# Kernel optimization log

Measured on AMD Instinct MI355X. Metric: run time of the kernel, lower is better.

Reference implementation:

```python
import jax, jax.numpy as jnp
import numpy as np

KQ = 512
NEG = -1e9


def setup_inputs() -> dict:
    key = jax.random.key(0)
    k1, k2, k3, k4, k5 = jax.random.split(key, 5)
    B, NQ, NK, D, V, O = 16, 1024, 2048, 512, 512, 256
    return {
        "keys": jax.random.normal(k1, (B, NK, D), dtype=jnp.float32),
        "queries": jax.random.normal(k2, (B, NQ, D), dtype=jnp.float32),
        "values": jax.random.normal(k3, (B, NK, V), dtype=jnp.float32),
        "mask": jax.random.randint(k4, (B, NQ, NK), 0, 2, dtype=jnp.int32),
        "W_resize": jax.random.normal(k5, (O, V), dtype=jnp.float32) * (1.0 / np.sqrt(V)),
        "b_resize": jnp.zeros((O,), dtype=jnp.float32),
    }


def reference(keys, queries, values, mask, W_resize, b_resize):
    # score: scaled dot product  [B, NQ, NK]
    logits = jnp.einsum("bqd,bkd->bqk", queries, keys) / jnp.sqrt(jnp.float32(KQ))
    logits = jnp.where(mask == 0, jnp.float32(NEG), logits)
    attn = jax.nn.softmax(logits, axis=-1)
    # context: [B, NQ, V]
    context = jnp.einsum("bqk,bkv->bqv", attn, values)
    # resize to out_size
    context = jnp.einsum("bqv,ov->bqo", context, W_resize) + b_resize
    return context
```

## Files before the change

### kernel.cpp

```cpp
#include <hip/hip_runtime.h>

#define BB   16
#define NQ   1024
#define NK   2048
#define DD   512
#define VV   512
#define OO   256
#define SCALE 0.044194173824159216f

typedef __attribute__((ext_vector_type(4))) float f32x4;
typedef __attribute__((ext_vector_type(8))) short s16x8;

#define AS1(p) ((const __attribute__((address_space(1))) void*)(p))
#define AS3(p) ((__attribute__((address_space(3))) void*)(p))

__device__ __forceinline__ unsigned short f2bf(float f) {
  unsigned u = __float_as_uint(f);
  u += 0x7fffu + ((u >> 16) & 1u);
  return (unsigned short)(u >> 16);
}
__device__ __forceinline__ float bf2f(unsigned short b) {
  return __uint_as_float(((unsigned)b) << 16);
}

#define MFMA16(a, b, c) __builtin_amdgcn_mfma_f32_16x16x32_bf16(a, b, c, 0, 0, 0)

__device__ __forceinline__ void gemm_bt_core(
    const unsigned short* __restrict__ Abase,
    const unsigned short* __restrict__ Bbase,
    int K,
    unsigned short* As, unsigned short* Bs,
    f32x4 acc[4][4])
{
  const int t = threadIdx.x;
  const int w = t >> 6;
  const int l = t & 63;
  const int srow = l >> 2;
  const int scol = (l & 3) * 8;
  const int r0 = (w * 2 + 0) * 16 + srow;
  const int r1 = (w * 2 + 1) * 16 + srow;
  const int lds0 = (w * 2 + 0) * 512 + l * 8;
  const int lds1 = (w * 2 + 1) * 512 + l * 8;
  const int wm = (w >> 1) * 64;
  const int wn = (w & 1) * 64;
  const int lm = l & 15;
  const int lq = l >> 4;

  for (int kt = 0; kt < K; kt += 32) {
    __builtin_amdgcn_global_load_lds(AS1(Abase + (size_t)r0 * K + kt + scol), AS3(As + lds0), 16, 0, 0);
    __builtin_amdgcn_global_load_lds(AS1(Abase + (size_t)r1 * K + kt + scol), AS3(As + lds1), 16, 0, 0);
    __builtin_amdgcn_global_load_lds(AS1(Bbase + (size_t)r0 * K + kt + scol), AS3(Bs + lds0), 16, 0, 0);
    __builtin_amdgcn_global_load_lds(AS1(Bbase + (size_t)r1 * K + kt + scol), AS3(Bs + lds1), 16, 0, 0);
    __syncthreads();
    s16x8 af[4], bfr[4];
    #pragma unroll
    for (int i = 0; i < 4; ++i) {
      af[i]  = *(const s16x8*)(As + (wm + i * 16 + lm) * 32 + lq * 8);
      bfr[i] = *(const s16x8*)(Bs + (wn + i * 16 + lm) * 32 + lq * 8);
    }
    #pragma unroll
    for (int mi = 0; mi < 4; ++mi)
      #pragma unroll
      for (int ni = 0; ni < 4; ++ni)
        acc[mi][ni] = MFMA16(af[mi], bfr[ni], acc[mi][ni]);
    __syncthreads();
  }
}


#define CS_STRIDE 136

__global__ __launch_bounds__(256)
void qkvw_kernel(const unsigned short* __restrict__ Qb,
                 const unsigned short* __restrict__ Kb,
                 const unsigned short* __restrict__ Vb,
                 const unsigned short* __restrict__ Wb,
                 const int* __restrict__ mask,
                 unsigned short* __restrict__ P,
                 unsigned short* __restrict__ VWt,
                 float* __restrict__ sums)
{
  __shared__ unsigned short smem[128 * CS_STRIDE];
  unsigned short* As = smem;
  unsigned short* Bs = smem + 4096;
  unsigned short* Cs = smem;
  const int bid = blockIdx.x;
  const int t = threadIdx.x, w = t >> 6, l = t & 63;
  const int wm = (w >> 1) * 64, wn = (w & 1) * 64;
  const int lm = l & 15, lq = l >> 4;
  const int trow = t >> 4, tcol = (t & 15) * 8;

  f32x4 acc[4][4];
  #pragma unroll
  for (int i = 0; i < 4; ++i)
    #pragma unroll
    for (int j = 0; j < 4; ++j) acc[i][j] = (f32x4){0.f, 0.f, 0.f, 0.f};

  if (bid < 2048) {
    const int b  = bid >> 7;
    const int tm = (bid >> 4) & 7;
    const int tn = bid & 15;

    gemm_bt_core(Qb + ((size_t)b * NQ + tm * 128) * DD,
                 Kb + ((size_t)b * NK + tn * 128) * DD, DD, As, Bs, acc);

    #pragma unroll
    for (int mi = 0; mi < 4; ++mi)
      #pragma unroll
      for (int ni = 0; ni < 4; ++ni)
        #pragma unroll
        for (int r = 0; r < 4; ++r)
          Cs[(wm + mi * 16 + lq * 4 + r) * CS_STRIDE + wn + ni * 16 + lm] =
              f2bf(acc[mi][ni][r] * SCALE);
    __syncthreads();

    #pragma unroll
    for (int it = 0; it < 8; ++it) {
      const int row = it * 16 + trow;
      const int gq = tm * 128 + row;
      const size_t gbase = ((size_t)b * NQ + gq) * NK + tn * 128 + tcol;
      s16x8 v = *(const s16x8*)(Cs + row * CS_STRIDE + tcol);
      const int4 m0 = *(const int4*)(mask + gbase);
      const int4 m1 = *(const int4*)(mask + gbase + 4);
      float e[8];
      e[0] = m0.x ? __expf(bf2f((unsigned short)v[0])) : 0.f;
      e[1] = m0.y ? __expf(bf2f((unsigned short)v[1])) : 0.f;
      e[2] = m0.z ? __expf(bf2f((unsigned short)v[2])) : 0.f;
      e[3] = m0.w ? __expf(bf2f((unsigned short)v[3])) : 0.f;
      e[4] = m1.x ? __expf(bf2f((unsigned short)v[4])) : 0.f;
      e[5] = m1.y ? __expf(bf2f((unsigned short)v[5])) : 0.f;
      e[6] = m1.z ? __expf(bf2f((unsigned short)v[6])) : 0.f;
      e[7] = m1.w ? __expf(bf2f((unsigned short)v[7])) : 0.f;
      float sp = 0.f;
      #pragma unroll
      for (int j = 0; j < 8; ++j) sp += e[j];
      #pragma unroll
      for (int off = 8; off > 0; off >>= 1) sp += __shfl_down(sp, off, 16);
      if ((t & 15) == 0) atomicAdd(&sums[(size_t)b * NQ + gq], sp);
      s16x8 o;
      #pragma unroll
      for (int j = 0; j < 8; ++j) o[j] = (short)f2bf(e[j]);
      *(s16x8*)(P + gbase) = o;
    }
  } else {
    const int vid = bid - 2048;
    const int b  = vid >> 5;
    const int kt = (vid >> 1) & 15;
    const int ot = vid & 1;

    gemm_bt_core(Vb + ((size_t)b * NK + kt * 128) * VV,
                 Wb + (size_t)ot * 128 * VV, VV, As, Bs, acc);

    #pragma unroll
    for (int mi = 0; mi < 4; ++mi)
      #pragma unroll
      for (int ni = 0; ni < 4; ++ni)
        #pragma unroll
        for (int r = 0; r < 4; ++r)
          Cs[(wn + ni * 16 + lm) * CS_STRIDE + wm + mi * 16 + lq * 4 + r] =
              f2bf(acc[mi][ni][r]);
    __syncthreads();

    #pragma unroll
    for (int it = 0; it < 8; ++it) {
      const int orow = it * 16 + trow;
      s16x8 v = *(const s16x8*)(Cs + orow * CS_STRIDE + tcol);
      *(s16x8*)(VWt + ((size_t)b * OO + ot * 128 + orow) * NK + kt * 128 + tcol) = v;
    }
  }
}

#define PW_STRIDE 132
__global__ __launch_bounds__(256)
void pvw_kernel(const unsigned short* __restrict__ P,
                const unsigned short* __restrict__ VWt,
                const float* __restrict__ sums,
                const float* __restrict__ bias,
                float* __restrict__ out)
{
  const int ot = blockIdx.x;
  const int qt = blockIdx.y;
  const int b  = blockIdx.z;
  __shared__ unsigned short smem[24576];
  __shared__ float Ls[64];

  const int t = threadIdx.x, w = t >> 6, l = t & 63;
  const int wr = w >> 1, wc = w & 1;
  const int lm = l & 15, lq = l >> 4;
  if (t < 64) Ls[t] = 1.0f / sums[(size_t)b * NQ + qt * 64 + t];

  f32x4 acc[2][4];
  #pragma unroll
  for (int i = 0; i < 2; ++i)
    #pragma unroll
    for (int j = 0; j < 4; ++j) acc[i][j] = (f32x4){0.f, 0.f, 0.f, 0.f};

  const unsigned short* Abase = P   + ((size_t)b * NQ + qt * 64) * NK;
  const unsigned short* Bbase = VWt + ((size_t)b * OO + ot * 128) * NK;

  const int srow = t >> 3;
  const int ssc  = (((t & 7) ^ (srow & 7)) << 3);

#define PV_STAGE(buf, k0v) do {                                                            \
    unsigned short* As_ = smem + (buf) * 12288;                                            \
    unsigned short* Bs_ = As_ + 4096;                                                      \
    const int k0_ = (k0v);                                                                 \
    __builtin_amdgcn_global_load_lds(AS1(Abase + (size_t)(srow     ) * NK + k0_ + ssc), AS3(As_ +        t * 8), 16, 0, 0); \
    __builtin_amdgcn_global_load_lds(AS1(Abase + (size_t)(srow + 32) * NK + k0_ + ssc), AS3(As_ + 2048 + t * 8), 16, 0, 0); \
    __builtin_amdgcn_global_load_lds(AS1(Bbase + (size_t)(srow     ) * NK + k0_ + ssc), AS3(Bs_ +        t * 8), 16, 0, 0); \
    __builtin_amdgcn_global_load_lds(AS1(Bbase + (size_t)(srow + 32) * NK + k0_ + ssc), AS3(Bs_ + 2048 + t * 8), 16, 0, 0); \
    __builtin_amdgcn_global_load_lds(AS1(Bbase + (size_t)(srow + 64) * NK + k0_ + ssc), AS3(Bs_ + 4096 + t * 8), 16, 0, 0); \
    __builtin_amdgcn_global_load_lds(AS1(Bbase + (size_t)(srow + 96) * NK + k0_ + ssc), AS3(Bs_ + 6144 + t * 8), 16, 0, 0); \
  } while (0)

  PV_STAGE(0, 0);
  __syncthreads();
  for (int k0 = 0; k0 < NK; k0 += 64) {
    const int cur = (k0 >> 6) & 1;
    if (k0 + 64 < NK) PV_STAGE(cur ^ 1, k0 + 64);
    const unsigned short* As = smem + cur * 12288;
    const unsigned short* Bs = As + 4096;
    s16x8 af[2][2], bfr[4][2];
    #pragma unroll
    for (int mi = 0; mi < 2; ++mi) {
      const int row = wr * 32 + mi * 16 + lm;
      #pragma unroll
      for (int ks = 0; ks < 2; ++ks)
        af[mi][ks] = *(const s16x8*)(As + row * 64 + (((ks * 4 + lq) ^ (row & 7)) << 3));
    }
    #pragma unroll
    for (int ni = 0; ni < 4; ++ni) {
      const int row = wc * 64 + ni * 16 + lm;
      #pragma unroll
      for (int ks = 0; ks < 2; ++ks)
        bfr[ni][ks] = *(const s16x8*)(Bs + row * 64 + (((ks * 4 + lq) ^ (row & 7)) << 3));
    }
    #pragma unroll
    for (int mi = 0; mi < 2; ++mi)
      #pragma unroll
      for (int ni = 0; ni < 4; ++ni) {
        acc[mi][ni] = MFMA16(af[mi][0], bfr[ni][0], acc[mi][ni]);
        acc[mi][ni] = MFMA16(af[mi][1], bfr[ni][1], acc[mi][ni]);
      }
    __syncthreads();
  }
#undef PV_STAGE

  float* Csf = (float*)smem;
  #pragma unroll
  for (int mi = 0; mi < 2; ++mi)
    #pragma unroll
    for (int ni = 0; ni < 4; ++ni)
      #pragma unroll
      for (int r = 0; r < 4; ++r) {
        const int row = wr * 32 + mi * 16 + lq * 4 + r;
        const int col = wc * 64 + ni * 16 + lm;
        Csf[row * PW_STRIDE + col] = acc[mi][ni][r] * Ls[row];
      }
  __syncthreads();
  const int trow = t >> 2;
  #pragma unroll
  for (int it = 0; it < 4; ++it) {
    const int col = (t & 3) * 8 + it * 32;
    f32x4 a = *(const f32x4*)(Csf + trow * PW_STRIDE + col);
    f32x4 c = *(const f32x4*)(Csf + trow * PW_STRIDE + col + 4);
    const int go = ot * 128 + col;
    a += *(const f32x4*)(bias + go);
    c += *(const f32x4*)(bias + go + 4);
    float* o = out + ((size_t)b * NQ + qt * 64 + trow) * OO + go;
    *(f32x4*)o = a;
    *(f32x4*)(o + 4) = c;
  }
}

__device__ __forceinline__ void cvt8(const float* __restrict__ in,
                                     unsigned short* __restrict__ out, int i)
{
  const float4* p = (const float4*)in + (size_t)i * 2;
  const float4 a = p[0], b = p[1];
  s16x8 o;
  o[0] = (short)f2bf(a.x); o[1] = (short)f2bf(a.y);
  o[2] = (short)f2bf(a.z); o[3] = (short)f2bf(a.w);
  o[4] = (short)f2bf(b.x); o[5] = (short)f2bf(b.y);
  o[6] = (short)f2bf(b.z); o[7] = (short)f2bf(b.w);
  ((s16x8*)out)[i] = o;
}

__global__ __launch_bounds__(256)
void prep_kernel(const float* __restrict__ q, const float* __restrict__ k,
                 const float* __restrict__ v, const float* __restrict__ w,
                 unsigned short* __restrict__ Qb, unsigned short* __restrict__ Kb,
                 unsigned short* __restrict__ Vb, unsigned short* __restrict__ Wb,
                 float* __restrict__ sums)
{
  const int bid = blockIdx.x;
  const int t = threadIdx.x;
  if (bid < 1024) {
    const int g0 = bid * 1024 + t;
    #pragma unroll
    for (int it = 0; it < 4; ++it) cvt8(q, Qb, g0 + it * 256);
  } else if (bid < 3072) {
    const int g0 = (bid - 1024) * 1024 + t;
    #pragma unroll
    for (int it = 0; it < 4; ++it) cvt8(k, Kb, g0 + it * 256);
  } else if (bid < 5120) {
    const int g0 = (bid - 3072) * 1024 + t;
    #pragma unroll
    for (int it = 0; it < 4; ++it) cvt8(v, Vb, g0 + it * 256);
  } else if (bid < 5136) {
    const int g0 = (bid - 5120) * 1024 + t;
    #pragma unroll
    for (int it = 0; it < 4; ++it) cvt8(w, Wb, g0 + it * 256);
  } else {
    const int i = (bid - 5136) * 1024 + t * 4;
    *(float4*)(sums + i) = (float4){0.f, 0.f, 0.f, 0.f};
  }
}

extern "C" void kernel_launch(void* const* d_in, const int* in_sizes, int n_in,
                              void* d_out, int out_size, void* d_ws, size_t ws_size,
                              hipStream_t stream)
{
  const float* keys    = (const float*)d_in[0];
  const float* queries = (const float*)d_in[1];
  const float* values  = (const float*)d_in[2];
  const int*   mask    = (const int*)  d_in[3];
  const float* W       = (const float*)d_in[4];
  const float* bias    = (const float*)d_in[5];
  float* out = (float*)d_out;

  char* ws = (char*)d_ws;
  unsigned short* Qb  = (unsigned short*)(ws);
  unsigned short* Kb  = (unsigned short*)(ws + (16ull << 20));
  unsigned short* Vb  = (unsigned short*)(ws + (48ull << 20));
  unsigned short* Wb  = (unsigned short*)(ws + (80ull << 20));
  unsigned short* VWt = (unsigned short*)(ws + (81ull << 20));
  unsigned short* P   = (unsigned short*)(ws + (97ull << 20));
  float* sums         = (float*)(ws + (161ull << 20));

  prep_kernel<<<dim3(5152), 256, 0, stream>>>(queries, keys, values, W,
                                              Qb, Kb, Vb, Wb, sums);
  qkvw_kernel<<<dim3(2560), 256, 0, stream>>>(Qb, Kb, Vb, Wb, mask, P, VWt, sums);
  pvw_kernel<<<dim3(OO / 128, NQ / 64, BB), 256, 0, stream>>>(P, VWt, sums, bias, out);
}
```

Measured before the change: 424.6 us.

## Compute softmax row sums via MFMA with ones vector instead of atomics

Drops the per-row atomicAdd of exp sums in the QK kernel, and the sums buffer with its zeroing. The PV kernel now computes the row sums itself with two extra MFMAs per k-step against a vector of bf16 ones. Because it sums the bf16-rounded P values, the normalisation matches what is actually multiplied. The change also remaps QK block indices into an XCD-interleaved order and splits the prep kernel into four times as many smaller blocks. The cost is extra MFMA work in PV, and the risk is a divide by zero when every key in a row is masked.

```diff
diff --git a/kernel.cpp b/kernel.cpp
--- a/kernel.cpp
+++ b/kernel.cpp
@@ -77,14 +77,14 @@
                  const unsigned short* __restrict__ Wb,
                  const int* __restrict__ mask,
                  unsigned short* __restrict__ P,
-                 unsigned short* __restrict__ VWt,
-                 float* __restrict__ sums)
+                 unsigned short* __restrict__ VWt)
 {
   __shared__ unsigned short smem[128 * CS_STRIDE];
   unsigned short* As = smem;
   unsigned short* Bs = smem + 4096;
   unsigned short* Cs = smem;
-  const int bid = blockIdx.x;
+  const int bid0 = blockIdx.x;
+  const int bid = (bid0 & 7) * 320 + (bid0 >> 3);
   const int t = threadIdx.x, w = t >> 6, l = t & 63;
   const int wm = (w >> 1) * 64, wn = (w & 1) * 64;
   const int lm = l & 15, lq = l >> 4;
@@ -122,24 +122,15 @@
       s16x8 v = *(const s16x8*)(Cs + row * CS_STRIDE + tcol);
       const int4 m0 = *(const int4*)(mask + gbase);
       const int4 m1 = *(const int4*)(mask + gbase + 4);
-      float e[8];
-      e[0] = m0.x ? __expf(bf2f((unsigned short)v[0])) : 0.f;
-      e[1] = m0.y ? __expf(bf2f((unsigned short)v[1])) : 0.f;
-      e[2] = m0.z ? __expf(bf2f((unsigned short)v[2])) : 0.f;
-      e[3] = m0.w ? __expf(bf2f((unsigned short)v[3])) : 0.f;
-      e[4] = m1.x ? __expf(bf2f((unsigned short)v[4])) : 0.f;
-      e[5] = m1.y ? __expf(bf2f((unsigned short)v[5])) : 0.f;
-      e[6] = m1.z ? __expf(bf2f((unsigned short)v[6])) : 0.f;
-      e[7] = m1.w ? __expf(bf2f((unsigned short)v[7])) : 0.f;
-      float sp = 0.f;
-      #pragma unroll
-      for (int j = 0; j < 8; ++j) sp += e[j];
-      #pragma unroll
-      for (int off = 8; off > 0; off >>= 1) sp += __shfl_down(sp, off, 16);
-      if ((t & 15) == 0) atomicAdd(&sums[(size_t)b * NQ + gq], sp);
       s16x8 o;
-      #pragma unroll
-      for (int j = 0; j < 8; ++j) o[j] = (short)f2bf(e[j]);
+      o[0] = m0.x ? (short)f2bf(__expf(bf2f((unsigned short)v[0]))) : (short)0;
+      o[1] = m0.y ? (short)f2bf(__expf(bf2f((unsigned short)v[1]))) : (short)0;
+      o[2] = m0.z ? (short)f2bf(__expf(bf2f((unsigned short)v[2]))) : (short)0;
+      o[3] = m0.w ? (short)f2bf(__expf(bf2f((unsigned short)v[3]))) : (short)0;
+      o[4] = m1.x ? (short)f2bf(__expf(bf2f((unsigned short)v[4]))) : (short)0;
+      o[5] = m1.y ? (short)f2bf(__expf(bf2f((unsigned short)v[5]))) : (short)0;
+      o[6] = m1.z ? (short)f2bf(__expf(bf2f((unsigned short)v[6]))) : (short)0;
+      o[7] = m1.w ? (short)f2bf(__expf(bf2f((unsigned short)v[7]))) : (short)0;
       *(s16x8*)(P + gbase) = o;
     }
   } else {
@@ -174,7 +165,6 @@
 __global__ __launch_bounds__(256)
 void pvw_kernel(const unsigned short* __restrict__ P,
                 const unsigned short* __restrict__ VWt,
-                const float* __restrict__ sums,
                 const float* __restrict__ bias,
                 float* __restrict__ out)
 {
@@ -182,18 +172,22 @@
   const int qt = blockIdx.y;
   const int b  = blockIdx.z;
   __shared__ unsigned short smem[24576];
-  __shared__ float Ls[64];
 
   const int t = threadIdx.x, w = t >> 6, l = t & 63;
   const int wr = w >> 1, wc = w & 1;
   const int lm = l & 15, lq = l >> 4;
-  if (t < 64) Ls[t] = 1.0f / sums[(size_t)b * NQ + qt * 64 + t];
 
   f32x4 acc[2][4];
   #pragma unroll
   for (int i = 0; i < 2; ++i)
     #pragma unroll
     for (int j = 0; j < 4; ++j) acc[i][j] = (f32x4){0.f, 0.f, 0.f, 0.f};
+  f32x4 accS[2];
+  accS[0] = (f32x4){0.f, 0.f, 0.f, 0.f};
+  accS[1] = (f32x4){0.f, 0.f, 0.f, 0.f};
+  s16x8 ones;
+  #pragma unroll
+  for (int j = 0; j < 8; ++j) ones[j] = (short)0x3F80;
 
   const unsigned short* Abase = P   + ((size_t)b * NQ + qt * 64) * NK;
   const unsigned short* Bbase = VWt + ((size_t)b * OO + ot * 128) * NK;
@@ -236,12 +230,15 @@
         bfr[ni][ks] = *(const s16x8*)(Bs + row * 64 + (((ks * 4 + lq) ^ (row & 7)) << 3));
     }
     #pragma unroll
-    for (int mi = 0; mi < 2; ++mi)
+    for (int mi = 0; mi < 2; ++mi) {
       #pragma unroll
       for (int ni = 0; ni < 4; ++ni) {
         acc[mi][ni] = MFMA16(af[mi][0], bfr[ni][0], acc[mi][ni]);
         acc[mi][ni] = MFMA16(af[mi][1], bfr[ni][1], acc[mi][ni]);
       }
+      accS[mi] = MFMA16(af[mi][0], ones, accS[mi]);
+      accS[mi] = MFMA16(af[mi][1], ones, accS[mi]);
+    }
     __syncthreads();
   }
 #undef PV_STAGE
@@ -250,13 +247,15 @@
   #pragma unroll
   for (int mi = 0; mi < 2; ++mi)
     #pragma unroll
-    for (int ni = 0; ni < 4; ++ni)
-      #pragma unroll
-      for (int r = 0; r < 4; ++r) {
-        const int row = wr * 32 + mi * 16 + lq * 4 + r;
+    for (int r = 0; r < 4; ++r) {
+      const float inv = 1.0f / accS[mi][r];
+      const int row = wr * 32 + mi * 16 + lq * 4 + r;
+      #pragma unroll
+      for (int ni = 0; ni < 4; ++ni) {
         const int col = wc * 64 + ni * 16 + lm;
-        Csf[row * PW_STRIDE + col] = acc[mi][ni][r] * Ls[row];
+        Csf[row * PW_STRIDE + col] = acc[mi][ni][r] * inv;
       }
+    }
   __syncthreads();
   const int trow = t >> 2;
   #pragma unroll
@@ -290,30 +289,18 @@
 void prep_kernel(const float* __restrict__ q, const float* __restrict__ k,
                  const float* __restrict__ v, const float* __restrict__ w,
                  unsigned short* __restrict__ Qb, unsigned short* __restrict__ Kb,
-                 unsigned short* __restrict__ Vb, unsigned short* __restrict__ Wb,
-                 float* __restrict__ sums)
+                 unsigned short* __restrict__ Vb, unsigned short* __restrict__ Wb)
 {
   const int bid = blockIdx.x;
   const int t = threadIdx.x;
-  if (bid < 1024) {
-    const int g0 = bid * 1024 + t;
-    #pragma unroll
-    for (int it = 0; it < 4; ++it) cvt8(q, Qb, g0 + it * 256);
-  } else if (bid < 3072) {
-    const int g0 = (bid - 1024) * 1024 + t;
-    #pragma unroll
-    for (int it = 0; it < 4; ++it) cvt8(k, Kb, g0 + it * 256);
-  } else if (bid < 5120) {
-    const int g0 = (bid - 3072) * 1024 + t;
-    #pragma unroll
-    for (int it = 0; it < 4; ++it) cvt8(v, Vb, g0 + it * 256);
-  } else if (bid < 5136) {
-    const int g0 = (bid - 5120) * 1024 + t;
-    #pragma unroll
-    for (int it = 0; it < 4; ++it) cvt8(w, Wb, g0 + it * 256);
+  if (bid < 4096) {
+    cvt8(q, Qb, bid * 256 + t);
+  } else if (bid < 12288) {
+    cvt8(k, Kb, (bid - 4096) * 256 + t);
+  } else if (bid < 20480) {
+    cvt8(v, Vb, (bid - 12288) * 256 + t);
   } else {
-    const int i = (bid - 5136) * 1024 + t * 4;
-    *(float4*)(sums + i) = (float4){0.f, 0.f, 0.f, 0.f};
+    cvt8(w, Wb, (bid - 20480) * 256 + t);
   }
 }
 
@@ -336,10 +323,9 @@
   unsigned short* Wb  = (unsigned short*)(ws + (80ull << 20));
   unsigned short* VWt = (unsigned short*)(ws + (81ull << 20));
   unsigned short* P   = (unsigned short*)(ws + (97ull << 20));
-  float* sums         = (float*)(ws + (161ull << 20));
-
-  prep_kernel<<<dim3(5152), 256, 0, stream>>>(queries, keys, values, W,
-                                              Qb, Kb, Vb, Wb, sums);
-  qkvw_kernel<<<dim3(2560), 256, 0, stream>>>(Qb, Kb, Vb, Wb, mask, P, VWt, sums);
-  pvw_kernel<<<dim3(OO / 128, NQ / 64, BB), 256, 0, stream>>>(P, VWt, sums, bias, out);
-}
+
+  prep_kernel<<<dim3(20544), 256, 0, stream>>>(queries, keys, values, W,
+                                               Qb, Kb, Vb, Wb);
+  qkvw_kernel<<<dim3(2560), 256, 0, stream>>>(Qb, Kb, Vb, Wb, mask, P, VWt);
+  pvw_kernel<<<dim3(OO / 128, NQ / 64, BB), 256, 0, stream>>>(P, VWt, bias, out);
+}
```

Result: faster. 413.8 us (-2.5%).
